# Kernel tuning notes

Hardware: AMD Instinct MI355X
Metric: run time of the kernel (lower is better)

## Reference

```python
import jax, jax.numpy as jnp
import numpy as np

B, S, I, H = 256, 512, 128, 256
THR = 0.001  # silence_threshold


def _glorot(k, shape):
    # xavier_uniform over the last two dims (matches nn.init.xavier_uniform_)
    fan_out, fan_in = shape[-2], shape[-1]
    lim = float(np.sqrt(6.0 / (fan_in + fan_out)))
    return jax.random.uniform(k, shape, jnp.float32, -lim, lim)


def setup_inputs() -> dict:
    key = jax.random.key(0)
    ks = jax.random.split(key, 8)
    # gate order along leading axis 0: [f, i, o, c]
    b_enc = jnp.concatenate([jnp.ones((1, H), jnp.float32), jnp.zeros((3, H), jnp.float32)], axis=0)
    return {
        "x": jax.random.normal(ks[0], (B, S, I), jnp.float32),
        # encoder: input->hidden and hidden->hidden weights (+ Linear biases + extra b_* params)
        "enc_Wx": _glorot(ks[1], (4, H, I)),
        "enc_bx": jnp.zeros((4, H), jnp.float32),
        "enc_Wh": _glorot(ks[2], (4, H, H)),
        "enc_bh": jnp.zeros((4, H), jnp.float32),
        "enc_b": b_enc,
        # decoder: its input_size == hidden_size
        "dec_Wx": _glorot(ks[3], (4, H, H)),
        "dec_bx": jnp.zeros((4, H), jnp.float32),
        "dec_Wh": _glorot(ks[4], (4, H, H)),
        "dec_bh": jnp.zeros((4, H), jnp.float32),
        "dec_b": b_enc,
        # reconstruct Linear(hidden_size -> input_size)
        "rec_W": _glorot(ks[5], (I, H)),
        "rec_b": jnp.zeros((I,), jnp.float32),
    }


def _cell(x, h, c, Wx, bx, Wh, bh, b):
    # fused gate GEMMs: g[k] = x @ Wx[k].T + bx[k] + h @ Wh[k].T + bh[k] + b[k]
    g = (jnp.einsum('bi,ghi->gbh', x, Wx) + bx[:, None, :]
         + jnp.einsum('bh,gkh->gbk', h, Wh) + bh[:, None, :]
         + b[:, None, :])  # [4, B, H]
    f_t = jax.nn.sigmoid(g[0])
    i_t = jax.nn.sigmoid(g[1])
    o_t = jax.nn.sigmoid(g[2])
    c_tilde = jnp.tanh(g[3])
    # silence mask on L2 norm over feature dim
    active = (jnp.linalg.norm(x, axis=1, keepdims=True) > THR).astype(x.dtype)
    c_next = f_t * c + i_t * c + active * (i_t * c_tilde)
    h_next = o_t * jnp.tanh(c_next)
    return h_next, c_next


def reference(x, enc_Wx, enc_bx, enc_Wh, enc_bh, enc_b,
              dec_Wx, dec_bx, dec_Wh, dec_bh, dec_b, rec_W, rec_b):
    Bsz, Slen = x.shape[0], x.shape[1]
    h0 = jnp.zeros((Bsz, H), x.dtype)
    c0 = jnp.zeros((Bsz, H), x.dtype)

    def enc_step(carry, xt):
        h, c = carry
        h, c = _cell(xt, h, c, enc_Wx, enc_bx, enc_Wh, enc_bh, enc_b)
        return (h, c), None

    (h_enc, c_enc), _ = jax.lax.scan(enc_step, (h0, c0), jnp.swapaxes(x, 0, 1))

    # in the decoder, decoder_input always equals h_prev (h fed back as input)
    def dec_step(carry, _):
        h, c = carry
        h, c = _cell(h, h, c, dec_Wx, dec_bx, dec_Wh, dec_bh, dec_b)
        out = h @ rec_W.T + rec_b  # [B, I]
        return (h, c), out

    _, outs = jax.lax.scan(dec_step, (h_enc, c_enc), None, length=Slen)
    return jnp.swapaxes(outs, 0, 1)  # [B, S, I]
```

## Files before the change

### kernel.cpp

```cpp
#include <hip/hip_runtime.h>
#include <cmath>

#define kB 256
#define kS 512
#define kI 128
#define kH 256

typedef __attribute__((ext_vector_type(8))) short short8;
typedef __attribute__((ext_vector_type(4))) float f32x4;
typedef unsigned long long u64;

#define AS_STRIDE 408

#define WS_HX_U64 (2 * 16 * 16 * 256)

__device__ __forceinline__ float sigmoidf_(float z) { return 1.0f / (1.0f + expf(-z)); }

__device__ __forceinline__ unsigned short f2b(float f) {
  unsigned u = __builtin_bit_cast(unsigned, f);
  unsigned r = (u + 0x7fffu + ((u >> 16) & 1u)) >> 16;
  return (unsigned short)r;
}
__device__ __forceinline__ float b2f(unsigned short s) {
  unsigned u = ((unsigned)s) << 16;
  return __builtin_bit_cast(float, u);
}
__device__ __forceinline__ void bsplit2(float f, unsigned short& h_, unsigned short& l_) {
  h_ = f2b(f);
  l_ = f2b(f - b2f(h_));
}
__device__ __forceinline__ void bsplit3(float f, unsigned short& h_, unsigned short& m_, unsigned short& l_) {
  h_ = f2b(f);
  float r1 = f - b2f(h_);
  m_ = f2b(r1);
  l_ = f2b(r1 - b2f(m_));
}

__device__ __forceinline__ void pollrow(const u64* grp, int tid, unsigned seq16, u64* u) {
  unsigned miss = 0xffffu;
  for (;;) {
    unsigned nm = 0;
#pragma unroll
    for (int j = 0; j < 16; ++j)
      if (miss & (1u << j))
        u[j] = __hip_atomic_load(grp + (size_t)j * 256 + tid, __ATOMIC_RELAXED, __HIP_MEMORY_SCOPE_SYSTEM);
#pragma unroll
    for (int j = 0; j < 16; ++j)
      if ((miss & (1u << j)) && (unsigned)(u[j] >> 48) != seq16) nm |= 1u << j;
    if (!nm) return;
    miss = nm;
    __builtin_amdgcn_s_sleep(1);
  }
}

__launch_bounds__(256, 1)
__global__ void lstm_mfma(const float* __restrict__ x,
                          const float* __restrict__ enc_Wx, const float* __restrict__ enc_bx,
                          const float* __restrict__ enc_Wh, const float* __restrict__ enc_bh,
                          const float* __restrict__ enc_b,
                          const float* __restrict__ dec_Wx, const float* __restrict__ dec_bx,
                          const float* __restrict__ dec_Wh, const float* __restrict__ dec_bh,
                          const float* __restrict__ dec_b,
                          const float* __restrict__ rec_W, const float* __restrict__ rec_b,
                          float* __restrict__ out,
                          u64* __restrict__ hx) {
  __shared__ __align__(16) short As_h[16 * AS_STRIDE];
  __shared__ __align__(16) short As_m[16 * AS_STRIDE];
  __shared__ __align__(16) short As_l[16 * AS_STRIDE];
  __shared__ float g_scr[4 * 16 * 17];
  __shared__ float r_scr[4 * 16 * 17];
  __shared__ float red[16][16];
  __shared__ float maskS[16];

  const int tid = threadIdx.x;
  const int bt = blockIdx.x & 15;
  const int ht = blockIdx.x >> 4;
  const int b0 = bt << 4, hh0 = ht << 4;
  const int w  = tid >> 6;
  const int l  = tid & 63;
  const int fr = l & 15;
  const int gq = l >> 4;
  const int b  = tid >> 4;
  const int q  = tid & 15;
  const int hh = hh0 + q;

  float be0 = enc_bx[0*kH+hh] + enc_bh[0*kH+hh] + enc_b[0*kH+hh];
  float be1 = enc_bx[1*kH+hh] + enc_bh[1*kH+hh] + enc_b[1*kH+hh];
  float be2 = enc_bx[2*kH+hh] + enc_bh[2*kH+hh] + enc_b[2*kH+hh];
  float be3 = enc_bx[3*kH+hh] + enc_bh[3*kH+hh] + enc_b[3*kH+hh];
  float bd0 = dec_bx[0*kH+hh] + dec_bh[0*kH+hh] + dec_b[0*kH+hh];
  float bd1 = dec_bx[1*kH+hh] + dec_bh[1*kH+hh] + dec_b[1*kH+hh];
  float bd2 = dec_bx[2*kH+hh] + dec_bh[2*kH+hh] + dec_b[2*kH+hh];
  float bd3 = dec_bx[3*kH+hh] + dec_bh[3*kH+hh] + dec_b[3*kH+hh];
  float recb = (ht < 8) ? rec_b[hh0 + q] : 0.0f;
  float creg = 0.0f;

  short8 wfh[12], wfm[12], wfl[12];
#pragma unroll
  for (int kst = 0; kst < 12; ++kst) {
    int k = kst * 32 + gq * 8;
    const float* src = (k < 128)
        ? (enc_Wx + ((size_t)(w * kH) + hh0 + fr) * kI + k)
        : (enc_Wh + ((size_t)(w * kH) + hh0 + fr) * kH + (k - 128));
    short8 hi, mi, lo;
#pragma unroll
    for (int j = 0; j < 8; ++j) {
      unsigned short h_, m_, l_;
      bsplit3(src[j], h_, m_, l_);
      hi[j] = (short)h_; mi[j] = (short)m_; lo[j] = (short)l_;
    }
    wfh[kst] = hi; wfm[kst] = mi; wfl[kst] = lo;
  }

  for (int s = 0; s < kS; ++s) {
    const int par = s & 1;
    if (q < 8) {
      const float* xp = x + ((size_t)(b0 + b) * kS + s) * kI + q * 16;
      float arr[16];
      *(float4*)(arr + 0)  = *(const float4*)(xp + 0);
      *(float4*)(arr + 4)  = *(const float4*)(xp + 4);
      *(float4*)(arr + 8)  = *(const float4*)(xp + 8);
      *(float4*)(arr + 12) = *(const float4*)(xp + 12);
      float ss = 0.f;
      short8 H0, H1, M0, M1, L0, L1;
#pragma unroll
      for (int j = 0; j < 16; ++j) {
        float v = arr[j];
        ss += v * v;
        unsigned short h_, m_, l_;
        bsplit3(v, h_, m_, l_);
        if (j < 8) { H0[j] = (short)h_; M0[j] = (short)m_; L0[j] = (short)l_; }
        else       { H1[j-8] = (short)h_; M1[j-8] = (short)m_; L1[j-8] = (short)l_; }
      }
      *(short8*)(As_h + b * AS_STRIDE + q * 16)     = H0;
      *(short8*)(As_h + b * AS_STRIDE + q * 16 + 8) = H1;
      *(short8*)(As_m + b * AS_STRIDE + q * 16)     = M0;
      *(short8*)(As_m + b * AS_STRIDE + q * 16 + 8) = M1;
      *(short8*)(As_l + b * AS_STRIDE + q * 16)     = L0;
      *(short8*)(As_l + b * AS_STRIDE + q * 16 + 8) = L1;
      red[b][q] = ss;
    }
    {
      const u64* grp = hx + ((size_t)(par * 16 + bt) * 16) * 256;
      u64 u[16];
      pollrow(grp, tid, (unsigned)(s & 0xffff), u);
#pragma unroll
      for (int j = 0; j < 16; ++j) {
        As_h[j * AS_STRIDE + 128 + tid] = (short)(unsigned short)(u[j] >> 32);
        As_m[j * AS_STRIDE + 128 + tid] = (short)(unsigned short)(u[j] >> 16);
        As_l[j * AS_STRIDE + 128 + tid] = (short)(unsigned short)(u[j]);
      }
    }
    __syncthreads();
    if (tid < 16) {
      float ss = 0.f;
#pragma unroll
      for (int j = 0; j < 8; ++j) ss += red[tid][j];
      maskS[tid] = (ss > 1e-6f) ? 1.0f : 0.0f;
    }
    f32x4 a0 = {0.f,0.f,0.f,0.f}, a1 = a0, a2 = a0, a3 = a0, a4 = a0, a5 = a0;
#pragma unroll
    for (int kst = 0; kst < 12; ++kst) {
      const short8 ah = *(const short8*)(As_h + fr * AS_STRIDE + kst * 32 + gq * 8);
      const short8 am = *(const short8*)(As_m + fr * AS_STRIDE + kst * 32 + gq * 8);
      const short8 al = *(const short8*)(As_l + fr * AS_STRIDE + kst * 32 + gq * 8);
      a0 = __builtin_amdgcn_mfma_f32_16x16x32_bf16(ah, wfh[kst], a0, 0, 0, 0);
      a1 = __builtin_amdgcn_mfma_f32_16x16x32_bf16(ah, wfm[kst], a1, 0, 0, 0);
      a2 = __builtin_amdgcn_mfma_f32_16x16x32_bf16(am, wfh[kst], a2, 0, 0, 0);
      a3 = __builtin_amdgcn_mfma_f32_16x16x32_bf16(ah, wfl[kst], a3, 0, 0, 0);
      a4 = __builtin_amdgcn_mfma_f32_16x16x32_bf16(am, wfm[kst], a4, 0, 0, 0);
      a5 = __builtin_amdgcn_mfma_f32_16x16x32_bf16(al, wfh[kst], a5, 0, 0, 0);
    }
    f32x4 d = (((a5 + a4) + a3) + (a2 + a1)) + a0;
#pragma unroll
    for (int i = 0; i < 4; ++i) g_scr[(w * 16 + gq * 4 + i) * 17 + fr] = d[i];
    __syncthreads();
    {
      float gf = g_scr[(0 * 16 + b) * 17 + q] + be0;
      float gi = g_scr[(1 * 16 + b) * 17 + q] + be1;
      float go = g_scr[(2 * 16 + b) * 17 + q] + be2;
      float gc = g_scr[(3 * 16 + b) * 17 + q] + be3;
      float m  = maskS[b];
      float f_ = sigmoidf_(gf), i_ = sigmoidf_(gi), o_ = sigmoidf_(go);
      float ct = tanhf(gc);
      creg = (f_ + i_) * creg + m * (i_ * ct);
      float hval = o_ * tanhf(creg);
      unsigned short hb, mb2, lb;
      bsplit3(hval, hb, mb2, lb);
      u64 pk = ((u64)(unsigned)((s + 1) & 0xffff) << 48) | ((u64)hb << 32) | ((u64)mb2 << 16) | (u64)lb;
      size_t wi = (((size_t)(((s + 1) & 1) * 16 + bt) * 16 + b) * 256) + hh0 + q;
      __hip_atomic_store(hx + wi, pk, __ATOMIC_RELAXED, __HIP_MEMORY_SCOPE_SYSTEM);
    }
  }

  short8 dwh[8], dwm[8], dwl[8];
#pragma unroll
  for (int kst = 0; kst < 8; ++kst) {
    int k = kst * 32 + gq * 8;
    const float* s1 = dec_Wx + ((size_t)(w * kH) + hh0 + fr) * kH + k;
    const float* s2 = dec_Wh + ((size_t)(w * kH) + hh0 + fr) * kH + k;
    short8 hi, mi, lo;
#pragma unroll
    for (int j = 0; j < 8; ++j) {
      unsigned short h_, m_, l_;
      bsplit3(s1[j] + s2[j], h_, m_, l_);
      hi[j] = (short)h_; mi[j] = (short)m_; lo[j] = (short)l_;
    }
    dwh[kst] = hi; dwm[kst] = mi; dwl[kst] = lo;
  }
  short8 rfh[2], rfl[2];
#pragma unroll
  for (int kk = 0; kk < 2; ++kk) {
    short8 hi = {0,0,0,0,0,0,0,0}, lo = hi;
    if (ht < 8) {
      int k = (2 * w + kk) * 32 + gq * 8;
      const float* src = rec_W + ((size_t)(hh0 + fr)) * kH + k;
#pragma unroll
      for (int j = 0; j < 8; ++j) {
        unsigned short h_, l_;
        bsplit2(src[j], h_, l_);
        hi[j] = (short)h_; lo[j] = (short)l_;
      }
    }
    rfh[kk] = hi; rfl[kk] = lo;
  }

  for (int t = 0; t < kS; ++t) {
    const int s = kS + t;
    const int par = s & 1;
    {
      const u64* grp = hx + ((size_t)(par * 16 + bt) * 16) * 256;
      u64 u[16];
      pollrow(grp, tid, (unsigned)(s & 0xffff), u);
#pragma unroll
      for (int j = 0; j < 16; ++j) {
        As_h[j * AS_STRIDE + tid] = (short)(unsigned short)(u[j] >> 32);
        As_m[j * AS_STRIDE + tid] = (short)(unsigned short)(u[j] >> 16);
        As_l[j * AS_STRIDE + tid] = (short)(unsigned short)(u[j]);
      }
    }
    __syncthreads();
    {
      float ss = 0.f;
#pragma unroll
      for (int g2 = 0; g2 < 2; ++g2) {
        const short8 hv = *(const short8*)(As_h + b * AS_STRIDE + q * 16 + g2 * 8);
        const short8 mv = *(const short8*)(As_m + b * AS_STRIDE + q * 16 + g2 * 8);
        const short8 lv = *(const short8*)(As_l + b * AS_STRIDE + q * 16 + g2 * 8);
#pragma unroll
        for (int j = 0; j < 8; ++j) {
          float v = b2f((unsigned short)hv[j]) + b2f((unsigned short)mv[j]) + b2f((unsigned short)lv[j]);
          ss += v * v;
        }
      }
      red[b][q] = ss;
    }
    __syncthreads();
    if (tid < 16) {
      float ss = 0.f;
#pragma unroll
      for (int j = 0; j < 16; ++j) ss += red[tid][j];
      maskS[tid] = (ss > 1e-6f) ? 1.0f : 0.0f;
    }
    f32x4 a0 = {0.f,0.f,0.f,0.f}, a1 = a0, a2 = a0, a3 = a0, a4 = a0, a5 = a0;
#pragma unroll
    for (int kst = 0; kst < 8; ++kst) {
      const short8 ah = *(const short8*)(As_h + fr * AS_STRIDE + kst * 32 + gq * 8);
      const short8 am = *(const short8*)(As_m + fr * AS_STRIDE + kst * 32 + gq * 8);
      const short8 al = *(const short8*)(As_l + fr * AS_STRIDE + kst * 32 + gq * 8);
      a0 = __builtin_amdgcn_mfma_f32_16x16x32_bf16(ah, dwh[kst], a0, 0, 0, 0);
      a1 = __builtin_amdgcn_mfma_f32_16x16x32_bf16(ah, dwm[kst], a1, 0, 0, 0);
      a2 = __builtin_amdgcn_mfma_f32_16x16x32_bf16(am, dwh[kst], a2, 0, 0, 0);
      a3 = __builtin_amdgcn_mfma_f32_16x16x32_bf16(ah, dwl[kst], a3, 0, 0, 0);
      a4 = __builtin_amdgcn_mfma_f32_16x16x32_bf16(am, dwm[kst], a4, 0, 0, 0);
      a5 = __builtin_amdgcn_mfma_f32_16x16x32_bf16(al, dwh[kst], a5, 0, 0, 0);
    }
    f32x4 d = (((a5 + a4) + a3) + (a2 + a1)) + a0;
#pragma unroll
    for (int i = 0; i < 4; ++i) g_scr[(w * 16 + gq * 4 + i) * 17 + fr] = d[i];
    if (ht < 8) {
      f32x4 r0 = {0.f,0.f,0.f,0.f}, r1 = r0, r2 = r0;
#pragma unroll
      for (int kk = 0; kk < 2; ++kk) {
        const short8 ah = *(const short8*)(As_h + fr * AS_STRIDE + (2 * w + kk) * 32 + gq * 8);
        const short8 am = *(const short8*)(As_m + fr * AS_STRIDE + (2 * w + kk) * 32 + gq * 8);
        r0 = __builtin_amdgcn_mfma_f32_16x16x32_bf16(ah, rfh[kk], r0, 0, 0, 0);
        r1 = __builtin_amdgcn_mfma_f32_16x16x32_bf16(ah, rfl[kk], r1, 0, 0, 0);
        r2 = __builtin_amdgcn_mfma_f32_16x16x32_bf16(am, rfh[kk], r2, 0, 0, 0);
      }
      f32x4 rd = r0 + r1 + r2;
#pragma unroll
      for (int i = 0; i < 4; ++i) r_scr[(w * 16 + gq * 4 + i) * 17 + fr] = rd[i];
    }
    __syncthreads();
    {
      float gf = g_scr[(0 * 16 + b) * 17 + q] + bd0;
      float gi = g_scr[(1 * 16 + b) * 17 + q] + bd1;
      float go = g_scr[(2 * 16 + b) * 17 + q] + bd2;
      float gc = g_scr[(3 * 16 + b) * 17 + q] + bd3;
      float m  = maskS[b];
      float f_ = sigmoidf_(gf), i_ = sigmoidf_(gi), o_ = sigmoidf_(go);
      float ct = tanhf(gc);
      creg = (f_ + i_) * creg + m * (i_ * ct);
      float hval = o_ * tanhf(creg);
      unsigned short hb, mb2, lb;
      bsplit3(hval, hb, mb2, lb);
      u64 pk = ((u64)(unsigned)((s + 1) & 0xffff) << 48) | ((u64)hb << 32) | ((u64)mb2 << 16) | (u64)lb;
      size_t wi = (((size_t)(((s + 1) & 1) * 16 + bt) * 16 + b) * 256) + hh0 + q;
      __hip_atomic_store(hx + wi, pk, __ATOMIC_RELAXED, __HIP_MEMORY_SCOPE_SYSTEM);
    }
    if (ht < 8 && t > 0) {
      float rsum = r_scr[(0 * 16 + b) * 17 + q] + r_scr[(1 * 16 + b) * 17 + q]
                 + r_scr[(2 * 16 + b) * 17 + q] + r_scr[(3 * 16 + b) * 17 + q] + recb;
      __builtin_nontemporal_store(rsum, &out[((size_t)(b0 + b) * kS + (t - 1)) * kI + hh0 + q]);
    }
  }

  {
    {
      const u64* grp = hx + ((size_t)(0 * 16 + bt) * 16) * 256;
      u64 u[16];
      pollrow(grp, tid, (unsigned)((2 * kS) & 0xffff), u);
#pragma unroll
      for (int j = 0; j < 16; ++j) {
        As_h[j * AS_STRIDE + tid] = (short)(unsigned short)(u[j] >> 32);
        As_m[j * AS_STRIDE + tid] = (short)(unsigned short)(u[j] >> 16);
      }
    }
    __syncthreads();
    if (ht < 8) {
      f32x4 r0 = {0.f,0.f,0.f,0.f}, r1 = r0, r2 = r0;
#pragma unroll
      for (int kk = 0; kk < 2; ++kk) {
        const short8 ah = *(const short8*)(As_h + fr * AS_STRIDE + (2 * w + kk) * 32 + gq * 8);
        const short8 am = *(const short8*)(As_m + fr * AS_STRIDE + (2 * w + kk) * 32 + gq * 8);
        r0 = __builtin_amdgcn_mfma_f32_16x16x32_bf16(ah, rfh[kk], r0, 0, 0, 0);
        r1 = __builtin_amdgcn_mfma_f32_16x16x32_bf16(ah, rfl[kk], r1, 0, 0, 0);
        r2 = __builtin_amdgcn_mfma_f32_16x16x32_bf16(am, rfh[kk], r2, 0, 0, 0);
      }
      f32x4 rd = r0 + r1 + r2;
#pragma unroll
      for (int i = 0; i < 4; ++i) r_scr[(w * 16 + gq * 4 + i) * 17 + fr] = rd[i];
    }
    __syncthreads();
    if (ht < 8) {
      float rsum = r_scr[(0 * 16 + b) * 17 + q] + r_scr[(1 * 16 + b) * 17 + q]
                 + r_scr[(2 * 16 + b) * 17 + q] + r_scr[(3 * 16 + b) * 17 + q] + recb;
      __builtin_nontemporal_store(rsum, &out[((size_t)(b0 + b) * kS + (kS - 1)) * kI + hh0 + q]);
    }
  }
}

extern "C" void kernel_launch(void* const* d_in, const int* in_sizes, int n_in,
                              void* d_out, int out_size, void* d_ws, size_t ws_size,
                              hipStream_t stream) {
  const float* x      = (const float*)d_in[0];
  const float* enc_Wx = (const float*)d_in[1];
  const float* enc_bx = (const float*)d_in[2];
  const float* enc_Wh = (const float*)d_in[3];
  const float* enc_bh = (const float*)d_in[4];
  const float* enc_b  = (const float*)d_in[5];
  const float* dec_Wx = (const float*)d_in[6];
  const float* dec_bx = (const float*)d_in[7];
  const float* dec_Wh = (const float*)d_in[8];
  const float* dec_bh = (const float*)d_in[9];
  const float* dec_b  = (const float*)d_in[10];
  const float* rec_W  = (const float*)d_in[11];
  const float* rec_b  = (const float*)d_in[12];
  float* out = (float*)d_out;

  u64* hx = (u64*)d_ws;

  hipMemsetAsync(d_ws, 0, (size_t)WS_HX_U64 * 8, stream);

  hipLaunchKernelGGL(lstm_mfma, dim3(256), dim3(256), 0, stream,
                     x, enc_Wx, enc_bx, enc_Wh, enc_bh, enc_b,
                     dec_Wx, dec_bx, dec_Wh, dec_bh, dec_b,
                     rec_W, rec_b, out, hx);
}
```

Measured before the change: 3.935 ms.

## Widen blocks to 512 threads covering 32 hidden columns to halve grid size

Each block now owns 32 hidden units (8 waves) instead of 16, and the grid shrinks from 256 to 128 blocks. The goal is to cut the number of blocks taking part in each step's cross-block spin-wait handshake on the shared h buffer, which is what limits this latency-bound recurrence. The per-step poll of h is split across the two 256-thread halves, 8 rows each. The gate and reconstruction scratch layouts are re-indexed to match. The launch bound of (512,2) caps registers per thread while each thread still holds 36 bf16 weight fragments, so register spills are a risk.

```diff
diff --git a/kernel.cpp b/kernel.cpp
--- a/kernel.cpp
+++ b/kernel.cpp
@@ -36,16 +36,18 @@
   l_ = f2b(r1 - b2f(m_));
 }
 
-__device__ __forceinline__ void pollrow(const u64* grp, int tid, unsigned seq16, u64* u) {
-  unsigned miss = 0xffffu;
+__device__ __forceinline__ void pollrow8(const u64* grp, int col, int rbase,
+                                         unsigned seq16, u64* u) {
+  unsigned miss = 0xffu;
   for (;;) {
     unsigned nm = 0;
 #pragma unroll
-    for (int j = 0; j < 16; ++j)
+    for (int j = 0; j < 8; ++j)
       if (miss & (1u << j))
-        u[j] = __hip_atomic_load(grp + (size_t)j * 256 + tid, __ATOMIC_RELAXED, __HIP_MEMORY_SCOPE_SYSTEM);
-#pragma unroll
-    for (int j = 0; j < 16; ++j)
+        u[j] = __hip_atomic_load(grp + (size_t)(rbase + j) * 256 + col,
+                                 __ATOMIC_RELAXED, __HIP_MEMORY_SCOPE_SYSTEM);
+#pragma unroll
+    for (int j = 0; j < 8; ++j)
       if ((miss & (1u << j)) && (unsigned)(u[j] >> 48) != seq16) nm |= 1u << j;
     if (!nm) return;
     miss = nm;
@@ -53,7 +55,7 @@
   }
 }
 
-__launch_bounds__(256, 1)
+__launch_bounds__(512, 2)
 __global__ void lstm_mfma(const float* __restrict__ x,
                           const float* __restrict__ enc_Wx, const float* __restrict__ enc_bx,
                           const float* __restrict__ enc_Wh, const float* __restrict__ enc_bh,
@@ -67,41 +69,45 @@
   __shared__ __align__(16) short As_h[16 * AS_STRIDE];
   __shared__ __align__(16) short As_m[16 * AS_STRIDE];
   __shared__ __align__(16) short As_l[16 * AS_STRIDE];
-  __shared__ float g_scr[4 * 16 * 17];
-  __shared__ float r_scr[4 * 16 * 17];
+  __shared__ float g_scr[8 * 16 * 17];
+  __shared__ float r_scr[8 * 16 * 17];
   __shared__ float red[16][16];
   __shared__ float maskS[16];
 
   const int tid = threadIdx.x;
   const int bt = blockIdx.x & 15;
   const int ht = blockIdx.x >> 4;
-  const int b0 = bt << 4, hh0 = ht << 4;
+  const int b0 = bt << 4, hh0 = ht << 5;
   const int w  = tid >> 6;
   const int l  = tid & 63;
   const int fr = l & 15;
   const int gq = l >> 4;
-  const int b  = tid >> 4;
-  const int q  = tid & 15;
-  const int hh = hh0 + q;
-
-  float be0 = enc_bx[0*kH+hh] + enc_bh[0*kH+hh] + enc_b[0*kH+hh];
-  float be1 = enc_bx[1*kH+hh] + enc_bh[1*kH+hh] + enc_b[1*kH+hh];
-  float be2 = enc_bx[2*kH+hh] + enc_bh[2*kH+hh] + enc_b[2*kH+hh];
-  float be3 = enc_bx[3*kH+hh] + enc_bh[3*kH+hh] + enc_b[3*kH+hh];
-  float bd0 = dec_bx[0*kH+hh] + dec_bh[0*kH+hh] + dec_b[0*kH+hh];
-  float bd1 = dec_bx[1*kH+hh] + dec_bh[1*kH+hh] + dec_b[1*kH+hh];
-  float bd2 = dec_bx[2*kH+hh] + dec_bh[2*kH+hh] + dec_b[2*kH+hh];
-  float bd3 = dec_bx[3*kH+hh] + dec_bh[3*kH+hh] + dec_b[3*kH+hh];
-  float recb = (ht < 8) ? rec_b[hh0 + q] : 0.0f;
+  const int cb = tid >> 5;
+  const int cq = tid & 31;
+  const int hhc = hh0 + cq;
+  const int col  = tid & 255;
+  const int rbase = (tid >> 8) * 8;
+
+  float be0 = enc_bx[0*kH+hhc] + enc_bh[0*kH+hhc] + enc_b[0*kH+hhc];
+  float be1 = enc_bx[1*kH+hhc] + enc_bh[1*kH+hhc] + enc_b[1*kH+hhc];
+  float be2 = enc_bx[2*kH+hhc] + enc_bh[2*kH+hhc] + enc_b[2*kH+hhc];
+  float be3 = enc_bx[3*kH+hhc] + enc_bh[3*kH+hhc] + enc_b[3*kH+hhc];
+  float bd0 = dec_bx[0*kH+hhc] + dec_bh[0*kH+hhc] + dec_b[0*kH+hhc];
+  float bd1 = dec_bx[1*kH+hhc] + dec_bh[1*kH+hhc] + dec_b[1*kH+hhc];
+  float bd2 = dec_bx[2*kH+hhc] + dec_bh[2*kH+hhc] + dec_b[2*kH+hhc];
+  float bd3 = dec_bx[3*kH+hhc] + dec_bh[3*kH+hhc] + dec_b[3*kH+hhc];
+  float recb = (ht < 4) ? rec_b[ht * 32 + cq] : 0.0f;
   float creg = 0.0f;
 
+  const int g  = w & 3;
+  const int hw = hh0 + ((w >> 2) << 4) + fr;
   short8 wfh[12], wfm[12], wfl[12];
 #pragma unroll
   for (int kst = 0; kst < 12; ++kst) {
     int k = kst * 32 + gq * 8;
     const float* src = (k < 128)
-        ? (enc_Wx + ((size_t)(w * kH) + hh0 + fr) * kI + k)
-        : (enc_Wh + ((size_t)(w * kH) + hh0 + fr) * kH + (k - 128));
+        ? (enc_Wx + ((size_t)(g * kH) + hw) * kI + k)
+        : (enc_Wh + ((size_t)(g * kH) + hw) * kH + (k - 128));
     short8 hi, mi, lo;
 #pragma unroll
     for (int j = 0; j < 8; ++j) {
@@ -114,8 +120,9 @@
 
   for (int s = 0; s < kS; ++s) {
     const int par = s & 1;
-    if (q < 8) {
-      const float* xp = x + ((size_t)(b0 + b) * kS + s) * kI + q * 16;
+    if (tid < 256 && (tid & 15) < 8) {
+      const int xb = tid >> 4, xq = tid & 15;
+      const float* xp = x + ((size_t)(b0 + xb) * kS + s) * kI + xq * 16;
       float arr[16];
       *(float4*)(arr + 0)  = *(const float4*)(xp + 0);
       *(float4*)(arr + 4)  = *(const float4*)(xp + 4);
@@ -132,23 +139,23 @@
         if (j < 8) { H0[j] = (short)h_; M0[j] = (short)m_; L0[j] = (short)l_; }
         else       { H1[j-8] = (short)h_; M1[j-8] = (short)m_; L1[j-8] = (short)l_; }
       }
-      *(short8*)(As_h + b * AS_STRIDE + q * 16)     = H0;
-      *(short8*)(As_h + b * AS_STRIDE + q * 16 + 8) = H1;
-      *(short8*)(As_m + b * AS_STRIDE + q * 16)     = M0;
-      *(short8*)(As_m + b * AS_STRIDE + q * 16 + 8) = M1;
-      *(short8*)(As_l + b * AS_STRIDE + q * 16)     = L0;
-      *(short8*)(As_l + b * AS_STRIDE + q * 16 + 8) = L1;
-      red[b][q] = ss;
+      *(short8*)(As_h + xb * AS_STRIDE + xq * 16)     = H0;
+      *(short8*)(As_h + xb * AS_STRIDE + xq * 16 + 8) = H1;
+      *(short8*)(As_m + xb * AS_STRIDE + xq * 16)     = M0;
+      *(short8*)(As_m + xb * AS_STRIDE + xq * 16 + 8) = M1;
+      *(short8*)(As_l + xb * AS_STRIDE + xq * 16)     = L0;
+      *(short8*)(As_l + xb * AS_STRIDE + xq * 16 + 8) = L1;
+      red[xb][xq] = ss;
     }
     {
       const u64* grp = hx + ((size_t)(par * 16 + bt) * 16) * 256;
-      u64 u[16];
-      pollrow(grp, tid, (unsigned)(s & 0xffff), u);
-#pragma unroll
-      for (int j = 0; j < 16; ++j) {
-        As_h[j * AS_STRIDE + 128 + tid] = (short)(unsigned short)(u[j] >> 32);
-        As_m[j * AS_STRIDE + 128 + tid] = (short)(unsigned short)(u[j] >> 16);
-        As_l[j * AS_STRIDE + 128 + tid] = (short)(unsigned short)(u[j]);
+      u64 u[8];
+      pollrow8(grp, col, rbase, (unsigned)(s & 0xffff), u);
+#pragma unroll
+      for (int j = 0; j < 8; ++j) {
+        As_h[(rbase + j) * AS_STRIDE + 128 + col] = (short)(unsigned short)(u[j] >> 32);
+        As_m[(rbase + j) * AS_STRIDE + 128 + col] = (short)(unsigned short)(u[j] >> 16);
+        As_l[(rbase + j) * AS_STRIDE + 128 + col] = (short)(unsigned short)(u[j]);
       }
     }
     __syncthreads();
@@ -176,11 +183,12 @@
     for (int i = 0; i < 4; ++i) g_scr[(w * 16 + gq * 4 + i) * 17 + fr] = d[i];
     __syncthreads();
     {
-      float gf = g_scr[(0 * 16 + b) * 17 + q] + be0;
-      float gi = g_scr[(1 * 16 + b) * 17 + q] + be1;
-      float go = g_scr[(2 * 16 + b) * 17 + q] + be2;
-      float gc = g_scr[(3 * 16 + b) * 17 + q] + be3;
-      float m  = maskS[b];
+      const int hsub = (cq >> 4) * 4, fq = cq & 15;
+      float gf = g_scr[((0 + hsub) * 16 + cb) * 17 + fq] + be0;
+      float gi = g_scr[((1 + hsub) * 16 + cb) * 17 + fq] + be1;
+      float go = g_scr[((2 + hsub) * 16 + cb) * 17 + fq] + be2;
+      float gc = g_scr[((3 + hsub) * 16 + cb) * 17 + fq] + be3;
+      float m  = maskS[cb];
       float f_ = sigmoidf_(gf), i_ = sigmoidf_(gi), o_ = sigmoidf_(go);
       float ct = tanhf(gc);
       creg = (f_ + i_) * creg + m * (i_ * ct);
@@ -188,7 +196,7 @@
       unsigned short hb, mb2, lb;
       bsplit3(hval, hb, mb2, lb);
       u64 pk = ((u64)(unsigned)((s + 1) & 0xffff) << 48) | ((u64)hb << 32) | ((u64)mb2 << 16) | (u64)lb;
-      size_t wi = (((size_t)(((s + 1) & 1) * 16 + bt) * 16 + b) * 256) + hh0 + q;
+      size_t wi = (((size_t)(((s + 1) & 1) * 16 + bt) * 16 + cb) * 256) + hhc;
       __hip_atomic_store(hx + wi, pk, __ATOMIC_RELAXED, __HIP_MEMORY_SCOPE_SYSTEM);
     }
   }
@@ -197,8 +205,8 @@
 #pragma unroll
   for (int kst = 0; kst < 8; ++kst) {
     int k = kst * 32 + gq * 8;
-    const float* s1 = dec_Wx + ((size_t)(w * kH) + hh0 + fr) * kH + k;
-    const float* s2 = dec_Wh + ((size_t)(w * kH) + hh0 + fr) * kH + k;
+    const float* s1 = dec_Wx + ((size_t)(g * kH) + hw) * kH + k;
+    const float* s2 = dec_Wh + ((size_t)(g * kH) + hw) * kH + k;
     short8 hi, mi, lo;
 #pragma unroll
     for (int j = 0; j < 8; ++j) {
@@ -212,9 +220,9 @@
 #pragma unroll
   for (int kk = 0; kk < 2; ++kk) {
     short8 hi = {0,0,0,0,0,0,0,0}, lo = hi;
-    if (ht < 8) {
-      int k = (2 * w + kk) * 32 + gq * 8;
-      const float* src = rec_W + ((size_t)(hh0 + fr)) * kH + k;
+    if (ht < 4) {
+      int k = (2 * (w & 3) + kk) * 32 + gq * 8;
+      const float* src = rec_W + ((size_t)(ht * 32 + ((w >> 2) << 4) + fr)) * kH + k;
 #pragma unroll
       for (int j = 0; j < 8; ++j) {
         unsigned short h_, l_;
@@ -230,30 +238,31 @@
     const int par = s & 1;
     {
       const u64* grp = hx + ((size_t)(par * 16 + bt) * 16) * 256;
-      u64 u[16];
-      pollrow(grp, tid, (unsigned)(s & 0xffff), u);
-#pragma unroll
-      for (int j = 0; j < 16; ++j) {
-        As_h[j * AS_STRIDE + tid] = (short)(unsigned short)(u[j] >> 32);
-        As_m[j * AS_STRIDE + tid] = (short)(unsigned short)(u[j] >> 16);
-        As_l[j * AS_STRIDE + tid] = (short)(unsigned short)(u[j]);
-      }
-    }
-    __syncthreads();
-    {
+      u64 u[8];
+      pollrow8(grp, col, rbase, (unsigned)(s & 0xffff), u);
+#pragma unroll
+      for (int j = 0; j < 8; ++j) {
+        As_h[(rbase + j) * AS_STRIDE + col] = (short)(unsigned short)(u[j] >> 32);
+        As_m[(rbase + j) * AS_STRIDE + col] = (short)(unsigned short)(u[j] >> 16);
+        As_l[(rbase + j) * AS_STRIDE + col] = (short)(unsigned short)(u[j]);
+      }
+    }
+    __syncthreads();
+    if (tid < 256) {
+      const int mb = tid >> 4, mq = tid & 15;
       float ss = 0.f;
 #pragma unroll
       for (int g2 = 0; g2 < 2; ++g2) {
-        const short8 hv = *(const short8*)(As_h + b * AS_STRIDE + q * 16 + g2 * 8);
-        const short8 mv = *(const short8*)(As_m + b * AS_STRIDE + q * 16 + g2 * 8);
-        const short8 lv = *(const short8*)(As_l + b * AS_STRIDE + q * 16 + g2 * 8);
+        const short8 hv = *(const short8*)(As_h + mb * AS_STRIDE + mq * 16 + g2 * 8);
+        const short8 mv = *(const short8*)(As_m + mb * AS_STRIDE + mq * 16 + g2 * 8);
+        const short8 lv = *(const short8*)(As_l + mb * AS_STRIDE + mq * 16 + g2 * 8);
 #pragma unroll
         for (int j = 0; j < 8; ++j) {
           float v = b2f((unsigned short)hv[j]) + b2f((unsigned short)mv[j]) + b2f((unsigned short)lv[j]);
           ss += v * v;
         }
       }
-      red[b][q] = ss;
+      red[mb][mq] = ss;
     }
     __syncthreads();
     if (tid < 16) {
@@ -278,12 +287,12 @@
     f32x4 d = (((a5 + a4) + a3) + (a2 + a1)) + a0;
 #pragma unroll
     for (int i = 0; i < 4; ++i) g_scr[(w * 16 + gq * 4 + i) * 17 + fr] = d[i];
-    if (ht < 8) {
+    if (ht < 4) {
       f32x4 r0 = {0.f,0.f,0.f,0.f}, r1 = r0, r2 = r0;
 #pragma unroll
       for (int kk = 0; kk < 2; ++kk) {
-        const short8 ah = *(const short8*)(As_h + fr * AS_STRIDE + (2 * w + kk) * 32 + gq * 8);
-        const short8 am = *(const short8*)(As_m + fr * AS_STRIDE + (2 * w + kk) * 32 + gq * 8);
+        const short8 ah = *(const short8*)(As_h + fr * AS_STRIDE + (2 * (w & 3) + kk) * 32 + gq * 8);
+        const short8 am = *(const short8*)(As_m + fr * AS_STRIDE + (2 * (w & 3) + kk) * 32 + gq * 8);
         r0 = __builtin_amdgcn_mfma_f32_16x16x32_bf16(ah, rfh[kk], r0, 0, 0, 0);
         r1 = __builtin_amdgcn_mfma_f32_16x16x32_bf16(ah, rfl[kk], r1, 0, 0, 0);
         r2 = __builtin_amdgcn_mfma_f32_16x16x32_bf16(am, rfh[kk], r2, 0, 0, 0);
@@ -294,11 +303,12 @@
     }
     __syncthreads();
     {
-      float gf = g_scr[(0 * 16 + b) * 17 + q] + bd0;
-      float gi = g_scr[(1 * 16 + b) * 17 + q] + bd1;
-      float go = g_scr[(2 * 16 + b) * 17 + q] + bd2;
-      float gc = g_scr[(3 * 16 + b) * 17 + q] + bd3;
-      float m  = maskS[b];
+      const int hsub = (cq >> 4) * 4, fq = cq & 15;
+      float gf = g_scr[((0 + hsub) * 16 + cb) * 17 + fq] + bd0;
+      float gi = g_scr[((1 + hsub) * 16 + cb) * 17 + fq] + bd1;
+      float go = g_scr[((2 + hsub) * 16 + cb) * 17 + fq] + bd2;
+      float gc = g_scr[((3 + hsub) * 16 + cb) * 17 + fq] + bd3;
+      float m  = maskS[cb];
       float f_ = sigmoidf_(gf), i_ = sigmoidf_(gi), o_ = sigmoidf_(go);
       float ct = tanhf(gc);
       creg = (f_ + i_) * creg + m * (i_ * ct);
@@ -306,34 +316,37 @@
       unsigned short hb, mb2, lb;
       bsplit3(hval, hb, mb2, lb);
       u64 pk = ((u64)(unsigned)((s + 1) & 0xffff) << 48) | ((u64)hb << 32) | ((u64)mb2 << 16) | (u64)lb;
-      size_t wi = (((size_t)(((s + 1) & 1) * 16 + bt) * 16 + b) * 256) + hh0 + q;
+      size_t wi = (((size_t)(((s + 1) & 1) * 16 + bt) * 16 + cb) * 256) + hhc;
       __hip_atomic_store(hx + wi, pk, __ATOMIC_RELAXED, __HIP_MEMORY_SCOPE_SYSTEM);
     }
-    if (ht < 8 && t > 0) {
-      float rsum = r_scr[(0 * 16 + b) * 17 + q] + r_scr[(1 * 16 + b) * 17 + q]
-                 + r_scr[(2 * 16 + b) * 17 + q] + r_scr[(3 * 16 + b) * 17 + q] + recb;
-      __builtin_nontemporal_store(rsum, &out[((size_t)(b0 + b) * kS + (t - 1)) * kI + hh0 + q]);
+    if (ht < 4 && t > 0) {
+      const int c2 = cq >> 4, fq = cq & 15;
+      float rsum = r_scr[((c2 * 4 + 0) * 16 + cb) * 17 + fq]
+                 + r_scr[((c2 * 4 + 1) * 16 + cb) * 17 + fq]
+                 + r_scr[((c2 * 4 + 2) * 16 + cb) * 17 + fq]
+                 + r_scr[((c2 * 4 + 3) * 16 + cb) * 17 + fq] + recb;
+      __builtin_nontemporal_store(rsum, &out[((size_t)(b0 + cb) * kS + (t - 1)) * kI + ht * 32 + cq]);
     }
   }
 
   {
     {
       const u64* grp = hx + ((size_t)(0 * 16 + bt) * 16) * 256;
-      u64 u[16];
-      pollrow(grp, tid, (unsigned)((2 * kS) & 0xffff), u);
-#pragma unroll
-      for (int j = 0; j < 16; ++j) {
-        As_h[j * AS_STRIDE + tid] = (short)(unsigned short)(u[j] >> 32);
-        As_m[j * AS_STRIDE + tid] = (short)(unsigned short)(u[j] >> 16);
-      }
-    }
-    __syncthreads();
-    if (ht < 8) {
+      u64 u[8];
+      pollrow8(grp, col, rbase, (unsigned)((2 * kS) & 0xffff), u);
+#pragma unroll
+      for (int j = 0; j < 8; ++j) {
+        As_h[(rbase + j) * AS_STRIDE + col] = (short)(unsigned short)(u[j] >> 32);
+        As_m[(rbase + j) * AS_STRIDE + col] = (short)(unsigned short)(u[j] >> 16);
+      }
+    }
+    __syncthreads();
+    if (ht < 4) {
       f32x4 r0 = {0.f,0.f,0.f,0.f}, r1 = r0, r2 = r0;
 #pragma unroll
       for (int kk = 0; kk < 2; ++kk) {
-        const short8 ah = *(const short8*)(As_h + fr * AS_STRIDE + (2 * w + kk) * 32 + gq * 8);
-        const short8 am = *(const short8*)(As_m + fr * AS_STRIDE + (2 * w + kk) * 32 + gq * 8);
+        const short8 ah = *(const short8*)(As_h + fr * AS_STRIDE + (2 * (w & 3) + kk) * 32 + gq * 8);
+        const short8 am = *(const short8*)(As_m + fr * AS_STRIDE + (2 * (w & 3) + kk) * 32 + gq * 8);
         r0 = __builtin_amdgcn_mfma_f32_16x16x32_bf16(ah, rfh[kk], r0, 0, 0, 0);
         r1 = __builtin_amdgcn_mfma_f32_16x16x32_bf16(ah, rfl[kk], r1, 0, 0, 0);
         r2 = __builtin_amdgcn_mfma_f32_16x16x32_bf16(am, rfh[kk], r2, 0, 0, 0);
@@ -343,10 +356,13 @@
       for (int i = 0; i < 4; ++i) r_scr[(w * 16 + gq * 4 + i) * 17 + fr] = rd[i];
     }
     __syncthreads();
-    if (ht < 8) {
-      float rsum = r_scr[(0 * 16 + b) * 17 + q] + r_scr[(1 * 16 + b) * 17 + q]
-                 + r_scr[(2 * 16 + b) * 17 + q] + r_scr[(3 * 16 + b) * 17 + q] + recb;
-      __builtin_nontemporal_store(rsum, &out[((size_t)(b0 + b) * kS + (kS - 1)) * kI + hh0 + q]);
+    if (ht < 4) {
+      const int c2 = cq >> 4, fq = cq & 15;
+      float rsum = r_scr[((c2 * 4 + 0) * 16 + cb) * 17 + fq]
+                 + r_scr[((c2 * 4 + 1) * 16 + cb) * 17 + fq]
+                 + r_scr[((c2 * 4 + 2) * 16 + cb) * 17 + fq]
+                 + r_scr[((c2 * 4 + 3) * 16 + cb) * 17 + fq] + recb;
+      __builtin_nontemporal_store(rsum, &out[((size_t)(b0 + cb) * kS + (kS - 1)) * kI + ht * 32 + cq]);
     }
   }
 }
@@ -373,7 +389,7 @@
 
   hipMemsetAsync(d_ws, 0, (size_t)WS_HX_U64 * 8, stream);
 
-  hipLaunchKernelGGL(lstm_mfma, dim3(256), dim3(256), 0, stream,
+  hipLaunchKernelGGL(lstm_mfma, dim3(128), dim3(512), 0, stream,
                      x, enc_Wx, enc_bx, enc_Wh, enc_bh, enc_b,
                      dec_Wx, dec_bx, dec_Wh, dec_bh, dec_b,
                      rec_W, rec_b, out, hx);
```

After: 3.755 ms, median of 2. 1.05x faster.
